# Kernel tuning notes

Hardware: AMD Instinct MI355X
Metric: run time of the kernel (lower is better)

Reference implementation:

```python
import jax, jax.numpy as jnp
import numpy as np

ALPHA = 0.2      # leak / integration time constant
E_FRAC = 0.8     # fraction of excitatory units (Dale's law)
NUM_LAYERS = 3


def setup_inputs() -> dict:
    key = jax.random.key(0)
    T, B, IN, H = 128, 64, 512, 1024
    ks = jax.random.split(key, 7)
    inputs = jax.random.normal(ks[0], (T, B, IN), jnp.float32)
    hidden_init = jax.random.uniform(ks[1], (1, B, H), jnp.float32) * 0.1
    # positive weights (clamped-positive in the original EI cell); Dale sign applied in reference
    W_in0 = jax.random.uniform(ks[2], (H, IN), jnp.float32) * (1.0 / np.sqrt(IN))
    W_in1 = jax.random.uniform(ks[3], (H, H), jnp.float32) * (1.0 / np.sqrt(H))
    W_in2 = jax.random.uniform(ks[4], (H, H), jnp.float32) * (1.0 / np.sqrt(H))
    W_rec = jax.random.uniform(ks[5], (NUM_LAYERS, H, H), jnp.float32) * (1.0 / H)
    b = jnp.zeros((NUM_LAYERS, H), jnp.float32)
    return {"inputs": inputs, "hidden_init": hidden_init, "W_in0": W_in0,
            "W_in1": W_in1, "W_in2": W_in2, "W_rec": W_rec, "b": b}


def reference(inputs, hidden_init, W_in0, W_in1, W_in2, W_rec, b):
    H = W_rec.shape[-1]
    ne = int(H * E_FRAC)
    signs = jnp.concatenate([jnp.ones((ne,), inputs.dtype), -jnp.ones((H - ne,), inputs.dtype)])
    e_mask = (signs > 0).astype(inputs.dtype)           # [H], zero out inhibitory feedforward
    # Dale's law: positive magnitudes with fixed presynaptic sign (columns)
    W_eff = jnp.abs(W_rec) * signs[None, None, :]        # [L, H, H]
    W_ins = (jnp.abs(W_in0), jnp.abs(W_in1), jnp.abs(W_in2))
    h0 = hidden_init[0]                                  # [B, H], shared across layers

    def step(carry, x_t):
        hs, vs = carry
        cell_input = x_t
        new_hs, new_vs = [], []
        for j in range(NUM_LAYERS):
            pre = cell_input @ W_ins[j].T + hs[j] @ W_eff[j].T + b[j]
            v = (1.0 - ALPHA) * vs[j] + ALPHA * pre      # leaky preact state
            h = jax.nn.relu(v)
            cell_input = h * e_mask                      # only excitatory units project forward
            new_hs.append(h)
            new_vs.append(v)
        return (tuple(new_hs), tuple(new_vs)), (cell_input, jnp.stack(new_hs))

    init = (tuple(h0 for _ in range(NUM_LAYERS)),
            tuple(jnp.zeros_like(h0) for _ in range(NUM_LAYERS)))
    _, (outputs, hiddens) = jax.lax.scan(step, init, inputs)
    # outputs: [T, B, H]; hiddens: [T, L, B, H] -> per-layer [T+1, B, H] incl. init
    hiddens = jnp.moveaxis(hiddens, 1, 0)                # [L, T, B, H]
    init_stack = jnp.broadcast_to(h0, (NUM_LAYERS, 1) + h0.shape)
    all_hiddens = jnp.concatenate([init_stack, hiddens], axis=1)  # [L, T+1, B, H]
    return outputs, all_hiddens
```

## Files before the change

### kernel.cpp

```cpp
#include <hip/hip_runtime.h>

#define T_STEPS 128
#define BATCH   64
#define INDIM   512
#define HDIM    1024
#define NE      819
#define OUT0_SZ (T_STEPS*BATCH*HDIM)
#define BH      (BATCH*HDIM)
#define ALLH_L  (129*BH)

#define HS_LAY   131072
#define HS_SLOT  393216
#define NSLOT    131
#define XF_T     65536
#define NBLK     192
#define NGRP     8
#define GSZ      24

typedef short bf16x8 __attribute__((ext_vector_type(8)));
typedef short short2v __attribute__((ext_vector_type(2)));
typedef float f32x4  __attribute__((ext_vector_type(4)));
typedef float f32x2  __attribute__((ext_vector_type(2)));

__device__ __forceinline__ short f2bf(float f){
    unsigned u = __float_as_uint(f);
    u += 0x7FFF + ((u >> 16) & 1);
    return (short)(u >> 16);
}
__device__ __forceinline__ float bf2f(short s){
    return __uint_as_float(((unsigned)(unsigned short)s) << 16);
}

__global__ __launch_bounds__(256) void ei_prep_w(const float* __restrict__ Win0,
        const float* __restrict__ Win1, const float* __restrict__ Win2,
        const float* __restrict__ Wrec, short* __restrict__ wf){
    int gid = blockIdx.x * 256 + threadIdx.x;
    int j, local, nkb, kff; const float* Win; short* base;
    if (gid < 196608)      { j=0; local=gid;        nkb=48; kff=512;  Win=Win0; base=wf; }
    else if (gid < 458752) { j=1; local=gid-196608; nkb=64; kff=1024; Win=Win1; base=wf+3145728; }
    else                   { j=2; local=gid-458752; nkb=64; kff=1024; Win=Win2; base=wf+7340032; }
    int lane = local & 63;
    int fi   = local >> 6;
    int kb   = fi % nkb;
    int it   = fi / nkb;
    int i    = it*16 + (lane & 15);
    int k0   = kb*32 + ((lane >> 4) << 3);
    const float* wrec_row = Wrec + ((size_t)j*HDIM + i)*HDIM;
    bf16x8 hv, lv;
    #pragma unroll
    for (int e = 0; e < 8; ++e){
        int k = k0 + e;
        float w;
        if (k < kff){
            w = fabsf(Win[(size_t)i*kff + k]);
            if (j != 0 && k >= NE) w = 0.f;
        } else {
            int kr = k - kff;
            w = fabsf(wrec_row[kr]);
            if (kr >= NE) w = -w;
        }
        short h = f2bf(w);
        hv[e] = h;
        lv[e] = f2bf(w - bf2f(h));
    }
    short* dst = base + (size_t)fi*1024 + lane*8;
    *(bf16x8*)dst         = hv;
    *(bf16x8*)(dst + 512) = lv;
}

__global__ __launch_bounds__(256) void ei_prep_xf(const float* __restrict__ x,
        short* __restrict__ xf){
    int gid = blockIdx.x * 256 + threadIdx.x;
    int lane = gid & 63;
    int bt   = (gid >> 6) & 3;
    int kb   = (gid >> 8) & 15;
    int t    = gid >> 12;
    int b = bt*16 + (lane & 15);
    int k = kb*32 + ((lane >> 4) << 3);
    const float* src = x + ((size_t)t*BATCH + b)*INDIM + k;
    float4 v0 = *(const float4*)src;
    float4 v1 = *(const float4*)(src + 4);
    float f[8] = {v0.x,v0.y,v0.z,v0.w,v1.x,v1.y,v1.z,v1.w};
    bf16x8 hv, lv;
    #pragma unroll
    for (int e = 0; e < 8; ++e){
        short h = f2bf(f[e]);
        hv[e] = h; lv[e] = f2bf(f[e] - bf2f(h));
    }
    short* dst = xf + (size_t)t*XF_T + (((size_t)(kb*4 + bt)) << 9) + lane*8;
    *(bf16x8*)dst            = hv;
    *(bf16x8*)(dst + 32768)  = lv;
}

__global__ __launch_bounds__(256) void ei_init5(const float* __restrict__ h0,
        float* __restrict__ out, short* __restrict__ hf, int* __restrict__ bar){
    int idx = blockIdx.x * 256 + threadIdx.x;
    int l = idx >> 16, r = idx & 0xFFFF;
    out[OUT0_SZ + (size_t)l*ALLH_L + r] = h0[r];
    if (idx < 1024) bar[idx] = 0;
    if (idx < 24576){
        int lane = idx & 63, bt = (idx >> 6) & 3, kb = (idx >> 8) & 31, j = idx >> 13;
        int b = bt*16 + (lane & 15);
        int k = kb*32 + ((lane >> 4) << 3);
        const float* src = h0 + (size_t)b*HDIM + k;
        float4 v0 = *(const float4*)src;
        float4 v1 = *(const float4*)(src + 4);
        float f[8] = {v0.x,v0.y,v0.z,v0.w,v1.x,v1.y,v1.z,v1.w};
        bf16x8 hv, lv;
        #pragma unroll
        for (int e = 0; e < 8; ++e){
            short hh = f2bf(f[e]);
            hv[e] = hh; lv[e] = f2bf(f[e] - bf2f(hh));
        }
        int off = ((kb*4 + bt) << 9) + lane*8;
        short* b0 = hf + (size_t)j*HS_LAY + off;
        *(bf16x8*)b0           = hv;
        *(bf16x8*)(b0 + 65536) = lv;
    }
}

template<int NKW, int NKFF, int FFLO>
__device__ __forceinline__ void step_mm4(
        const short* __restrict__ pff, const short* __restrict__ prec,
        const short* __restrict__ wp0, const short* __restrict__ wp1,
        int kb0, int btbase, int laneo, f32x4 acc[2][2])
{
    bf16x8 ah[NKW][2], al[NKW][2];
    #pragma unroll
    for (int kk = 0; kk < NKW; ++kk){
        int kb = kb0 + kk;
        const short* pa; int lo;
        if (kb < NKFF){ pa = pff + (kb << 11); lo = FFLO; }
        else          { pa = prec + ((kb - NKFF) << 11); lo = 65536; }
        ah[kk][0] = *(const bf16x8*)(pa + ((btbase + 0) << 9) + laneo);
        ah[kk][1] = *(const bf16x8*)(pa + ((btbase + 1) << 9) + laneo);
        al[kk][0] = *(const bf16x8*)(pa + lo + ((btbase + 0) << 9) + laneo);
        al[kk][1] = *(const bf16x8*)(pa + lo + ((btbase + 1) << 9) + laneo);
    }
    __builtin_amdgcn_sched_barrier(0);
    bf16x8 wh[2][2], wl[2][2];
    {
        const short* a = wp0 + (kb0 << 10);
        const short* b = wp1 + (kb0 << 10);
        wh[0][0] = *(const bf16x8*)a; wl[0][0] = *(const bf16x8*)(a + 512);
        wh[0][1] = *(const bf16x8*)b; wl[0][1] = *(const bf16x8*)(b + 512);
    }
    __builtin_amdgcn_sched_barrier(0);
    #pragma unroll
    for (int kk = 0; kk < NKW; ++kk){
        if (kk + 1 < NKW){
            const int nb = (kk + 1) & 1;
            const short* a = wp0 + ((kb0 + kk + 1) << 10);
            const short* b = wp1 + ((kb0 + kk + 1) << 10);
            wh[nb][0] = *(const bf16x8*)a; wl[nb][0] = *(const bf16x8*)(a + 512);
            wh[nb][1] = *(const bf16x8*)b; wl[nb][1] = *(const bf16x8*)(b + 512);
        }
        const int b2 = kk & 1;
        acc[0][0] = __builtin_amdgcn_mfma_f32_16x16x32_bf16(ah[kk][0], wh[b2][0], acc[0][0], 0,0,0);
        acc[0][1] = __builtin_amdgcn_mfma_f32_16x16x32_bf16(ah[kk][1], wh[b2][0], acc[0][1], 0,0,0);
        acc[1][0] = __builtin_amdgcn_mfma_f32_16x16x32_bf16(ah[kk][0], wh[b2][1], acc[1][0], 0,0,0);
        acc[1][1] = __builtin_amdgcn_mfma_f32_16x16x32_bf16(ah[kk][1], wh[b2][1], acc[1][1], 0,0,0);
        acc[0][0] = __builtin_amdgcn_mfma_f32_16x16x32_bf16(al[kk][0], wh[b2][0], acc[0][0], 0,0,0);
        acc[0][1] = __builtin_amdgcn_mfma_f32_16x16x32_bf16(al[kk][1], wh[b2][0], acc[0][1], 0,0,0);
        acc[1][0] = __builtin_amdgcn_mfma_f32_16x16x32_bf16(al[kk][0], wh[b2][1], acc[1][0], 0,0,0);
        acc[1][1] = __builtin_amdgcn_mfma_f32_16x16x32_bf16(al[kk][1], wh[b2][1], acc[1][1], 0,0,0);
        acc[0][0] = __builtin_amdgcn_mfma_f32_16x16x32_bf16(ah[kk][0], wl[b2][0], acc[0][0], 0,0,0);
        acc[0][1] = __builtin_amdgcn_mfma_f32_16x16x32_bf16(ah[kk][1], wl[b2][0], acc[0][1], 0,0,0);
        acc[1][0] = __builtin_amdgcn_mfma_f32_16x16x32_bf16(ah[kk][0], wl[b2][1], acc[1][0], 0,0,0);
        acc[1][1] = __builtin_amdgcn_mfma_f32_16x16x32_bf16(ah[kk][1], wl[b2][1], acc[1][1], 0,0,0);
    }
}

__global__ __launch_bounds__(512, 2) void ei_persist7(
        const short* __restrict__ xf, const short* __restrict__ wf,
        const float* __restrict__ bias, float* __restrict__ out,
        short* __restrict__ hf, int* __restrict__ bar)
{
    const int bid   = blockIdx.x;
    const int g     = bid & 7;
    const int w     = bid >> 3;
    const int j     = w >> 3;
    const int strip = g*4 + ((w >> 1) & 3);
    const int bhalf = w & 1;
    const int grp   = g;

    const int tx    = threadIdx.x;
    const int wv    = tx >> 6, lane = tx & 63;
    const int laneo = lane * 8;
    const int btbase = bhalf * 2;
    const int it0   = strip * 2;

    const short* wfj = wf + (j == 0 ? 0 : (j == 1 ? 3145728 : 7340032));
    const int nkb  = (j == 0) ? 48 : 64;
    const int NKW  = nkb >> 3;
    const int kb0  = wv * NKW;
    const short* wp0 = wfj + it0*nkb*1024 + laneo;
    const short* wp1 = wp0 + nkb*1024;

    const int btl = tx >> 8;
    const int q   = tx & 255;
    const int lnw = q >> 2;
    const int e0  = (q & 3) * 2;
    const int b_g = (bhalf*2 + btl)*16 + (lnw & 15);
    const int i_g = strip*32 + ((lnw >> 4) << 3) + e0;
    const int bl  = b_g & 31;
    const int il0 = ((lnw >> 4) << 3) + e0;
    const int hoff = ((strip*4 + bhalf*2 + btl) << 9) + q*2;
    const f32x2 bb = *(const f32x2*)&bias[j*HDIM + i_g];
    f32x2 vreg = {0.f, 0.f};

    __shared__ float psum[8][32][34];

    for (int s = 0; s < T_STEPS + 2; ++s){
        const int t = s - j;
        const bool act = (t >= 0) && (t < T_STEPS);
        if (s > 0){
            while (__hip_atomic_load(&bar[512 + grp*32],
                    __ATOMIC_RELAXED, __HIP_MEMORY_SCOPE_AGENT) < s)
                __builtin_amdgcn_s_sleep(1);
            asm volatile("" ::: "memory");
            __builtin_amdgcn_sched_barrier(0);
        }
        if (act){
            const short* hfr  = hf + (size_t)s*HS_SLOT;
            const short* prec = (t == 0) ? (hf + (size_t)j*HS_LAY)
                                         : (hfr + (size_t)j*HS_LAY);
            f32x4 acc[2][2] = {{{0.f,0.f,0.f,0.f},{0.f,0.f,0.f,0.f}},
                               {{0.f,0.f,0.f,0.f},{0.f,0.f,0.f,0.f}}};
            if (j == 0)
                step_mm4<6,16,32768>(xf + (size_t)t*XF_T, prec, wp0, wp1, kb0, btbase, laneo, acc);
            else if (j == 1)
                step_mm4<8,32,65536>(hfr, prec, wp0, wp1, kb0, btbase, laneo, acc);
            else
                step_mm4<8,32,65536>(hfr + HS_LAY, prec, wp0, wp1, kb0, btbase, laneo, acc);

            const int r0 = (lane >> 4) << 2, l15 = lane & 15;
            #pragma unroll
            for (int ic = 0; ic < 2; ++ic)
                #pragma unroll
                for (int bt = 0; bt < 2; ++bt)
                    #pragma unroll
                    for (int r = 0; r < 4; ++r)
                        psum[wv][bt*16 + r0 + r][ic*16 + l15] = acc[ic][bt][r];
        }
        __syncthreads();
        if (act){
            float sum0 = 0.f, sum1 = 0.f;
            #pragma unroll
            for (int ww = 0; ww < 8; ++ww){
                f32x2 p = *(f32x2*)&psum[ww][bl][il0];
                sum0 += p[0]; sum1 += p[1];
            }
            vreg[0] = 0.8f*vreg[0] + 0.2f*(sum0 + bb[0]);
            vreg[1] = 0.8f*vreg[1] + 0.2f*(sum1 + bb[1]);
            float h0v = vreg[0] > 0.f ? vreg[0] : 0.f;
            float h1v = vreg[1] > 0.f ? vreg[1] : 0.f;
            f32x2 hv2 = {h0v, h1v};
            *(f32x2*)&out[OUT0_SZ + ((size_t)(j*129 + t + 1))*BH + b_g*HDIM + i_g] = hv2;
            if (j == 2){
                f32x2 o2 = {(i_g < NE) ? h0v : 0.f, (i_g + 1 < NE) ? h1v : 0.f};
                *(f32x2*)&out[(size_t)t*BH + b_g*HDIM + i_g] = o2;
            }
            short hh0 = f2bf(h0v), hl0 = f2bf(h0v - bf2f(hh0));
            short hh1 = f2bf(h1v), hl1 = f2bf(h1v - bf2f(hh1));
            int hi2 = (int)(unsigned short)hh0 | ((int)(unsigned short)hh1 << 16);
            int lo2 = (int)(unsigned short)hl0 | ((int)(unsigned short)hl1 << 16);
            short* hww = hf + (size_t)(s + 1)*HS_SLOT + (size_t)j*HS_LAY + hoff;
            asm volatile("global_store_dword %0, %1, off sc0 sc1"
                         :: "v"(hww), "v"(hi2) : "memory");
            asm volatile("global_store_dword %0, %1, off sc0 sc1"
                         :: "v"(hww + 65536), "v"(lo2) : "memory");
        }
        if (s == T_STEPS + 1) break;
        asm volatile("s_waitcnt vmcnt(0)" ::: "memory");
        __syncthreads();
        if (tx == 0){
            int prev = __hip_atomic_fetch_add(&bar[grp*32], 1,
                        __ATOMIC_RELAXED, __HIP_MEMORY_SCOPE_AGENT);
            if (prev == (s + 1)*GSZ - 1){
                int sp = __hip_atomic_fetch_add(&bar[256], 1,
                        __ATOMIC_RELAXED, __HIP_MEMORY_SCOPE_AGENT);
                if (sp == (s + 1)*NGRP - 1){
                    #pragma unroll
                    for (int gg = 0; gg < NGRP; ++gg)
                        __hip_atomic_store(&bar[512 + gg*32], s + 1,
                                __ATOMIC_RELAXED, __HIP_MEMORY_SCOPE_AGENT);
                }
            }
        }
    }
}

#define HS_PAR_FB 393216
__global__ __launch_bounds__(256) void ei_init3(const float* __restrict__ h0,
        float* __restrict__ out, float* __restrict__ v_ws, short* __restrict__ hfb){
    int idx = blockIdx.x * 256 + threadIdx.x;
    int l = idx >> 16, r = idx & 0xFFFF;
    float h = h0[r];
    out[OUT0_SZ + (size_t)l*ALLH_L + r] = h;
    v_ws[idx] = 0.f;
    if (idx < 24576){
        int lane = idx & 63, bt = (idx >> 6) & 3, kb = (idx >> 8) & 31, j = idx >> 13;
        int b = bt*16 + (lane & 15);
        int k = kb*32 + ((lane >> 4) << 3);
        const float* src = h0 + (size_t)b*HDIM + k;
        float4 v0 = *(const float4*)src;
        float4 v1 = *(const float4*)(src + 4);
        float f[8] = {v0.x,v0.y,v0.z,v0.w,v1.x,v1.y,v1.z,v1.w};
        bf16x8 hv, lv;
        #pragma unroll
        for (int e = 0; e < 8; ++e){
            short hh = f2bf(f[e]);
            hv[e] = hh; lv[e] = f2bf(f[e] - bf2f(hh));
        }
        int off = ((kb*4 + bt) << 9) + lane*8;
        short* b0 = hfb + (size_t)j*HS_LAY + off;
        *(bf16x8*)b0           = hv;
        *(bf16x8*)(b0 + 65536) = lv;
        short* b1 = b0 + HS_PAR_FB;
        *(bf16x8*)b1           = hv;
        *(bf16x8*)(b1 + 65536) = lv;
    }
}

template<int NKW, int NKFF, int FFLO>
__device__ __forceinline__ void stage_body5(
        const short* __restrict__ pff, const short* __restrict__ prec,
        const short* __restrict__ wp, int kb0, int laneo, f32x4 acc[4])
{
    bf16x8 wbh[NKW], wbl[NKW];
    #pragma unroll
    for (int kk = 0; kk < NKW; ++kk){
        const short* w0 = wp + ((kb0 + kk) << 10);
        wbh[kk] = *(const bf16x8*)w0;
        wbl[kk] = *(const bf16x8*)(w0 + 512);
    }
    bf16x8 ah[2][4], al[2][4];
    auto loadA = [&](int kk, int buf){
        int kb = kb0 + kk;
        const short* pa; int lo;
        if (kb < NKFF){ pa = pff + (kb << 11); lo = FFLO; }
        else          { pa = prec + ((kb - NKFF) << 11); lo = 65536; }
        #pragma unroll
        for (int bt = 0; bt < 4; ++bt){
            ah[buf][bt] = *(const bf16x8*)(pa + (bt << 9) + laneo);
            al[buf][bt] = *(const bf16x8*)(pa + lo + (bt << 9) + laneo);
        }
    };
    loadA(0, 0);
    #pragma unroll
    for (int kk = 0; kk < NKW; ++kk){
        if (kk + 1 < NKW) loadA(kk + 1, (kk + 1) & 1);
        const int bf = kk & 1;
        #pragma unroll
        for (int bt = 0; bt < 4; ++bt)
            acc[bt] = __builtin_amdgcn_mfma_f32_16x16x32_bf16(ah[bf][bt], wbh[kk], acc[bt], 0,0,0);
        #pragma unroll
        for (int bt = 0; bt < 4; ++bt)
            acc[bt] = __builtin_amdgcn_mfma_f32_16x16x32_bf16(al[bf][bt], wbh[kk], acc[bt], 0,0,0);
        #pragma unroll
        for (int bt = 0; bt < 4; ++bt)
            acc[bt] = __builtin_amdgcn_mfma_f32_16x16x32_bf16(ah[bf][bt], wbl[kk], acc[bt], 0,0,0);
    }
}

__global__ __launch_bounds__(512, 2) void ei_stage5(
        const short* __restrict__ xf, const short* __restrict__ wf,
        const float* __restrict__ bias, float* __restrict__ out,
        float* __restrict__ v_ws, short* __restrict__ hfb, int s)
{
    int j = blockIdx.x >> 6;
    int t = s - j;
    if (t < 0 || t >= T_STEPS) return;
    int it = blockIdx.x & 63;
    int wv = threadIdx.x >> 6, lane = threadIdx.x & 63;
    int laneo = lane * 8;
    int par_r = (s - 1) & 1, par_w = s & 1;
    const short* hfr  = hfb + par_r*HS_PAR_FB;
    const short* prec = hfr + j*HS_LAY;

    f32x4 acc[4] = {{0.f,0.f,0.f,0.f},{0.f,0.f,0.f,0.f},
                    {0.f,0.f,0.f,0.f},{0.f,0.f,0.f,0.f}};

    if (j == 0){
        const short* pff = xf + t*XF_T;
        const short* wp  = wf + it*48*1024 + laneo;
        stage_body5<6,16,32768>(pff, prec, wp, wv*6, laneo, acc);
    } else if (j == 1){
        const short* pff = hfr;
        const short* wp  = wf + 3145728 + it*64*1024 + laneo;
        stage_body5<8,32,65536>(pff, prec, wp, wv*8, laneo, acc);
    } else {
        const short* pff = hfr + HS_LAY;
        const short* wp  = wf + 7340032 + it*64*1024 + laneo;
        stage_body5<8,32,65536>(pff, prec, wp, wv*8, laneo, acc);
    }

    __shared__ float psum[8][64][18];
    {
        int r0 = (lane >> 4) << 2, l15 = lane & 15;
        #pragma unroll
        for (int bt = 0; bt < 4; ++bt)
            #pragma unroll
            for (int r = 0; r < 4; ++r)
                psum[wv][bt*16 + r0 + r][l15] = acc[bt][r];
    }
    __syncthreads();

    int tx  = threadIdx.x;
    int b   = tx >> 3;
    int il0 = (tx & 7) << 1;
    float* allh = out + OUT0_SZ + ((size_t)(j*129 + t + 1))*BH;
    float* outp = out + (size_t)t*BH;
    short* hww  = hfb + par_w*HS_PAR_FB + j*HS_LAY;
    float sum0 = 0.f, sum1 = 0.f;
    #pragma unroll
    for (int w = 0; w < 8; ++w){
        f32x2 p = *(f32x2*)&psum[w][b][il0];
        sum0 += p[0]; sum1 += p[1];
    }
    int i = it*16 + il0;
    f32x2 bb = *(const f32x2*)&bias[j*HDIM + i];
    int vo = (j*BATCH + b)*HDIM + i;
    f32x2 vold = *(f32x2*)&v_ws[vo];
    float vn0 = 0.8f * vold[0] + 0.2f * (sum0 + bb[0]);
    float vn1 = 0.8f * vold[1] + 0.2f * (sum1 + bb[1]);
    f32x2 vnv = {vn0, vn1};
    *(f32x2*)&v_ws[vo] = vnv;
    float h0 = vn0 > 0.f ? vn0 : 0.f;
    float h1 = vn1 > 0.f ? vn1 : 0.f;
    f32x2 hv2 = {h0, h1};
    *(f32x2*)&allh[b*HDIM + i] = hv2;
    short hh0 = f2bf(h0), hl0 = f2bf(h0 - bf2f(hh0));
    short hh1 = f2bf(h1), hl1 = f2bf(h1 - bf2f(hh1));
    int kb  = i >> 5, btw = b >> 4;
    int lnw = (b & 15) + (((i >> 3) & 3) << 4);
    int off = ((kb*4 + btw) << 9) + lnw*8 + (i & 7);
    short2v hi2 = {hh0, hh1}, lo2 = {hl0, hl1};
    *(short2v*)(hww + off)         = hi2;
    *(short2v*)(hww + off + 65536) = lo2;
    if (j == 2){
        f32x2 o2 = {(i < NE) ? h0 : 0.f, (i + 1 < NE) ? h1 : 0.f};
        *(f32x2*)&outp[b*HDIM + i] = o2;
    }
}

extern "C" void kernel_launch(void* const* d_in, const int* in_sizes, int n_in,
                              void* d_out, int out_size, void* d_ws, size_t ws_size,
                              hipStream_t stream) {
    const float* xin  = (const float*)d_in[0];
    const float* h0   = (const float*)d_in[1];
    const float* Win0 = (const float*)d_in[2];
    const float* Win1 = (const float*)d_in[3];
    const float* Win2 = (const float*)d_in[4];
    const float* Wrec = (const float*)d_in[5];
    const float* bias = (const float*)d_in[6];
    float* out  = (float*)d_out;
    char* ws    = (char*)d_ws;

    const size_t HF_B   = (size_t)NSLOT * HS_SLOT * 2ULL;
    const size_t need_p = 65536 + HF_B + 16777216ULL + 23068672ULL;

    if (ws_size >= need_p) {
        int*   bar = (int*)ws;
        short* hf  = (short*)(ws + 65536);
        short* xf  = (short*)(ws + 65536 + HF_B);
        short* wfp = (short*)(ws + 65536 + HF_B + 16777216ULL);
        hipLaunchKernelGGL(ei_prep_w, dim3(2816), dim3(256), 0, stream,
                           Win0, Win1, Win2, Wrec, wfp);
        hipLaunchKernelGGL(ei_prep_xf, dim3(2048), dim3(256), 0, stream, xin, xf);
        hipLaunchKernelGGL(ei_init5, dim3(768), dim3(256), 0, stream, h0, out, hf, bar);
        hipLaunchKernelGGL(ei_persist7, dim3(NBLK), dim3(512), 0, stream,
                           xf, wfp, bias, out, hf, bar);
    } else {
        float* v_ws = (float*)ws;
        short* hfb  = (short*)(ws + 786432);
        short* xf   = (short*)(ws + 786432 + 1572864ULL);
        short* wfp  = (short*)(ws + 786432 + 1572864ULL + 16777216ULL);
        hipLaunchKernelGGL(ei_prep_w, dim3(2816), dim3(256), 0, stream,
                           Win0, Win1, Win2, Wrec, wfp);
        hipLaunchKernelGGL(ei_prep_xf, dim3(2048), dim3(256), 0, stream, xin, xf);
        hipLaunchKernelGGL(ei_init3, dim3(768), dim3(256), 0, stream, h0, out, v_ws, hfb);
        for (int s = 0; s < T_STEPS + 2; ++s)
            hipLaunchKernelGGL(ei_stage5, dim3(192), dim3(512), 0, stream,
                               xf, wfp, bias, out, v_ws, hfb, s);
    }
}
```

Baseline: 1.082 ms.

## Double per-block output tile to 64 columns and halve persistent grid to 96 blocks

Each persistent block now computes 64 hidden columns (four 16-wide MFMA tiles) instead of 32, so the activation fragments loaded per k-step are reused across four weight tiles. The grid shrinks from 192 to 96 blocks and barrier group sizes are adjusted to match. The A-operand loads move from a full upfront preload to a double-buffered pipeline interleaved with the weight loads. The intent is to cut redundant activation traffic and reduce the number of blocks participating in each grid-wide barrier, at the cost of fewer CUs doing the per-step GEMM, more registers per thread and a larger shared reduction buffer. A leftover dead code block computes unused values.

```diff
diff --git a/kernel.cpp b/kernel.cpp
--- a/kernel.cpp
+++ b/kernel.cpp
@@ -13,9 +13,8 @@
 #define HS_SLOT  393216
 #define NSLOT    131
 #define XF_T     65536
-#define NBLK     192
-#define NGRP     8
-#define GSZ      24
+#define NBLK8    96
+#define GSZ8     12
 
 typedef short bf16x8 __attribute__((ext_vector_type(8)));
 typedef short short2v __attribute__((ext_vector_type(2)));
@@ -120,58 +119,48 @@
 }
 
 template<int NKW, int NKFF, int FFLO>
-__device__ __forceinline__ void step_mm4(
+__device__ __forceinline__ void step_mm8(
         const short* __restrict__ pff, const short* __restrict__ prec,
-        const short* __restrict__ wp0, const short* __restrict__ wp1,
-        int kb0, int btbase, int laneo, f32x4 acc[2][2])
+        const short* __restrict__ wp0, int wstride,
+        int kb0, int btbase, int laneo, f32x4 acc[4][2])
 {
-    bf16x8 ah[NKW][2], al[NKW][2];
-    #pragma unroll
-    for (int kk = 0; kk < NKW; ++kk){
+    bf16x8 wh[2][4], wl[2][4], ah[2][2], al[2][2];
+    auto loadW = [&](int kk, int buf){
+        #pragma unroll
+        for (int ic = 0; ic < 4; ++ic){
+            const short* a = wp0 + ic*wstride + ((kb0 + kk) << 10);
+            wh[buf][ic] = *(const bf16x8*)a;
+            wl[buf][ic] = *(const bf16x8*)(a + 512);
+        }
+    };
+    auto loadA = [&](int kk, int buf){
         int kb = kb0 + kk;
         const short* pa; int lo;
         if (kb < NKFF){ pa = pff + (kb << 11); lo = FFLO; }
         else          { pa = prec + ((kb - NKFF) << 11); lo = 65536; }
-        ah[kk][0] = *(const bf16x8*)(pa + ((btbase + 0) << 9) + laneo);
-        ah[kk][1] = *(const bf16x8*)(pa + ((btbase + 1) << 9) + laneo);
-        al[kk][0] = *(const bf16x8*)(pa + lo + ((btbase + 0) << 9) + laneo);
-        al[kk][1] = *(const bf16x8*)(pa + lo + ((btbase + 1) << 9) + laneo);
-    }
-    __builtin_amdgcn_sched_barrier(0);
-    bf16x8 wh[2][2], wl[2][2];
-    {
-        const short* a = wp0 + (kb0 << 10);
-        const short* b = wp1 + (kb0 << 10);
-        wh[0][0] = *(const bf16x8*)a; wl[0][0] = *(const bf16x8*)(a + 512);
-        wh[0][1] = *(const bf16x8*)b; wl[0][1] = *(const bf16x8*)(b + 512);
-    }
-    __builtin_amdgcn_sched_barrier(0);
+        ah[buf][0] = *(const bf16x8*)(pa + ((btbase + 0) << 9) + laneo);
+        ah[buf][1] = *(const bf16x8*)(pa + ((btbase + 1) << 9) + laneo);
+        al[buf][0] = *(const bf16x8*)(pa + lo + ((btbase + 0) << 9) + laneo);
+        al[buf][1] = *(const bf16x8*)(pa + lo + ((btbase + 1) << 9) + laneo);
+    };
+    loadW(0, 0); loadA(0, 0);
     #pragma unroll
     for (int kk = 0; kk < NKW; ++kk){
-        if (kk + 1 < NKW){
-            const int nb = (kk + 1) & 1;
-            const short* a = wp0 + ((kb0 + kk + 1) << 10);
-            const short* b = wp1 + ((kb0 + kk + 1) << 10);
-            wh[nb][0] = *(const bf16x8*)a; wl[nb][0] = *(const bf16x8*)(a + 512);
-            wh[nb][1] = *(const bf16x8*)b; wl[nb][1] = *(const bf16x8*)(b + 512);
-        }
-        const int b2 = kk & 1;
-        acc[0][0] = __builtin_amdgcn_mfma_f32_16x16x32_bf16(ah[kk][0], wh[b2][0], acc[0][0], 0,0,0);
-        acc[0][1] = __builtin_amdgcn_mfma_f32_16x16x32_bf16(ah[kk][1], wh[b2][0], acc[0][1], 0,0,0);
-        acc[1][0] = __builtin_amdgcn_mfma_f32_16x16x32_bf16(ah[kk][0], wh[b2][1], acc[1][0], 0,0,0);
-        acc[1][1] = __builtin_amdgcn_mfma_f32_16x16x32_bf16(ah[kk][1], wh[b2][1], acc[1][1], 0,0,0);
-        acc[0][0] = __builtin_amdgcn_mfma_f32_16x16x32_bf16(al[kk][0], wh[b2][0], acc[0][0], 0,0,0);
-        acc[0][1] = __builtin_amdgcn_mfma_f32_16x16x32_bf16(al[kk][1], wh[b2][0], acc[0][1], 0,0,0);
-        acc[1][0] = __builtin_amdgcn_mfma_f32_16x16x32_bf16(al[kk][0], wh[b2][1], acc[1][0], 0,0,0);
-        acc[1][1] = __builtin_amdgcn_mfma_f32_16x16x32_bf16(al[kk][1], wh[b2][1], acc[1][1], 0,0,0);
-        acc[0][0] = __builtin_amdgcn_mfma_f32_16x16x32_bf16(ah[kk][0], wl[b2][0], acc[0][0], 0,0,0);
-        acc[0][1] = __builtin_amdgcn_mfma_f32_16x16x32_bf16(ah[kk][1], wl[b2][0], acc[0][1], 0,0,0);
-        acc[1][0] = __builtin_amdgcn_mfma_f32_16x16x32_bf16(ah[kk][0], wl[b2][1], acc[1][0], 0,0,0);
-        acc[1][1] = __builtin_amdgcn_mfma_f32_16x16x32_bf16(ah[kk][1], wl[b2][1], acc[1][1], 0,0,0);
-    }
-}
-
-__global__ __launch_bounds__(512, 2) void ei_persist7(
+        if (kk + 1 < NKW){ loadW(kk + 1, (kk + 1) & 1); loadA(kk + 1, (kk + 1) & 1); }
+        const int b = kk & 1;
+        #pragma unroll
+        for (int ic = 0; ic < 4; ++ic){
+            acc[ic][0] = __builtin_amdgcn_mfma_f32_16x16x32_bf16(ah[b][0], wh[b][ic], acc[ic][0], 0,0,0);
+            acc[ic][1] = __builtin_amdgcn_mfma_f32_16x16x32_bf16(ah[b][1], wh[b][ic], acc[ic][1], 0,0,0);
+            acc[ic][0] = __builtin_amdgcn_mfma_f32_16x16x32_bf16(al[b][0], wh[b][ic], acc[ic][0], 0,0,0);
+            acc[ic][1] = __builtin_amdgcn_mfma_f32_16x16x32_bf16(al[b][1], wh[b][ic], acc[ic][1], 0,0,0);
+            acc[ic][0] = __builtin_amdgcn_mfma_f32_16x16x32_bf16(ah[b][0], wl[b][ic], acc[ic][0], 0,0,0);
+            acc[ic][1] = __builtin_amdgcn_mfma_f32_16x16x32_bf16(ah[b][1], wl[b][ic], acc[ic][1], 0,0,0);
+        }
+    }
+}
+
+__global__ __launch_bounds__(512, 2) void ei_persist8(
         const short* __restrict__ xf, const short* __restrict__ wf,
         const float* __restrict__ bias, float* __restrict__ out,
         short* __restrict__ hf, int* __restrict__ bar)
@@ -179,8 +168,8 @@
     const int bid   = blockIdx.x;
     const int g     = bid & 7;
     const int w     = bid >> 3;
-    const int j     = w >> 3;
-    const int strip = g*4 + ((w >> 1) & 3);
+    const int j     = w >> 2;
+    const int strip = g*2 + ((w >> 1) & 1);
     const int bhalf = w & 1;
     const int grp   = g;
 
@@ -188,28 +177,31 @@
     const int wv    = tx >> 6, lane = tx & 63;
     const int laneo = lane * 8;
     const int btbase = bhalf * 2;
-    const int it0   = strip * 2;
+    const int it0   = strip * 4;
 
     const short* wfj = wf + (j == 0 ? 0 : (j == 1 ? 3145728 : 7340032));
     const int nkb  = (j == 0) ? 48 : 64;
     const int NKW  = nkb >> 3;
     const int kb0  = wv * NKW;
-    const short* wp0 = wfj + it0*nkb*1024 + laneo;
-    const short* wp1 = wp0 + nkb*1024;
-
-    const int btl = tx >> 8;
+    const int wstride = nkb * 1024;
+    const short* wp0 = wfj + it0*wstride + laneo;
+
+    const int c0  = tx >> 8;
     const int q   = tx & 255;
     const int lnw = q >> 2;
     const int e0  = (q & 3) * 2;
-    const int b_g = (bhalf*2 + btl)*16 + (lnw & 15);
-    const int i_g = strip*32 + ((lnw >> 4) << 3) + e0;
+    const int b_g = (bhalf*2 + c0)*16 + (lnw & 15);
     const int bl  = b_g & 31;
-    const int il0 = ((lnw >> 4) << 3) + e0;
-    const int hoff = ((strip*4 + bhalf*2 + btl) << 9) + q*2;
-    const f32x2 bb = *(const f32x2*)&bias[j*HDIM + i_g];
-    f32x2 vreg = {0.f, 0.f};
-
-    __shared__ float psum[8][32][34];
+    const int ilb = ((lnw >> 4) << 3) + e0;
+    const int i_g0 = strip*64 + ilb;
+    const int i_g1 = i_g0 + 32;
+    const int hoff0 = (((strip*2 + 0)*4 + bhalf*2 + c0) << 9) + q*2;
+    const int hoff1 = (((strip*2 + 1)*4 + bhalf*2 + c0) << 9) + q*2;
+    const f32x2 bb0 = *(const f32x2*)&bias[j*HDIM + i_g0];
+    const f32x2 bb1 = *(const f32x2*)&bias[j*HDIM + i_g1];
+    f32x2 vreg0 = {0.f, 0.f}, vreg1 = {0.f, 0.f};
+
+    __shared__ float psum[8][32][68];
 
     for (int s = 0; s < T_STEPS + 2; ++s){
         const int t = s - j;
@@ -225,18 +217,20 @@
             const short* hfr  = hf + (size_t)s*HS_SLOT;
             const short* prec = (t == 0) ? (hf + (size_t)j*HS_LAY)
                                          : (hfr + (size_t)j*HS_LAY);
-            f32x4 acc[2][2] = {{{0.f,0.f,0.f,0.f},{0.f,0.f,0.f,0.f}},
+            f32x4 acc[4][2] = {{{0.f,0.f,0.f,0.f},{0.f,0.f,0.f,0.f}},
+                               {{0.f,0.f,0.f,0.f},{0.f,0.f,0.f,0.f}},
+                               {{0.f,0.f,0.f,0.f},{0.f,0.f,0.f,0.f}},
                                {{0.f,0.f,0.f,0.f},{0.f,0.f,0.f,0.f}}};
             if (j == 0)
-                step_mm4<6,16,32768>(xf + (size_t)t*XF_T, prec, wp0, wp1, kb0, btbase, laneo, acc);
+                step_mm8<6,16,32768>(xf + (size_t)t*XF_T, prec, wp0, wstride, kb0, btbase, laneo, acc);
             else if (j == 1)
-                step_mm4<8,32,65536>(hfr, prec, wp0, wp1, kb0, btbase, laneo, acc);
+                step_mm8<8,32,65536>(hfr, prec, wp0, wstride, kb0, btbase, laneo, acc);
             else
-                step_mm4<8,32,65536>(hfr + HS_LAY, prec, wp0, wp1, kb0, btbase, laneo, acc);
+                step_mm8<8,32,65536>(hfr + HS_LAY, prec, wp0, wstride, kb0, btbase, laneo, acc);
 
             const int r0 = (lane >> 4) << 2, l15 = lane & 15;
             #pragma unroll
-            for (int ic = 0; ic < 2; ++ic)
+            for (int ic = 0; ic < 4; ++ic)
                 #pragma unroll
                 for (int bt = 0; bt < 2; ++bt)
                     #pragma unroll
@@ -245,31 +239,55 @@
         }
         __syncthreads();
         if (act){
-            float sum0 = 0.f, sum1 = 0.f;
+            float s00 = 0.f, s01 = 0.f, s10 = 0.f, s11 = 0.f;
             #pragma unroll
             for (int ww = 0; ww < 8; ++ww){
-                f32x2 p = *(f32x2*)&psum[ww][bl][il0];
-                sum0 += p[0]; sum1 += p[1];
+                f32x2 p0 = *(f32x2*)&psum[ww][bl][ilb];
+                f32x2 p1 = *(f32x2*)&psum[ww][bl][ilb + 32];
+                s00 += p0[0]; s01 += p0[1];
+                s10 += p1[0]; s11 += p1[1];
             }
-            vreg[0] = 0.8f*vreg[0] + 0.2f*(sum0 + bb[0]);
-            vreg[1] = 0.8f*vreg[1] + 0.2f*(sum1 + bb[1]);
-            float h0v = vreg[0] > 0.f ? vreg[0] : 0.f;
-            float h1v = vreg[1] > 0.f ? vreg[1] : 0.f;
-            f32x2 hv2 = {h0v, h1v};
-            *(f32x2*)&out[OUT0_SZ + ((size_t)(j*129 + t + 1))*BH + b_g*HDIM + i_g] = hv2;
+            vreg0[0] = 0.8f*vreg0[0] + 0.2f*(s00 + bb0[0]);
+            vreg0[1] = 0.8f*vreg0[1] + 0.2f*(s01 + bb0[1]);
+            vreg1[0] = 0.8f*vreg1[0] + 0.2f*(s10 + bb1[0]);
+            vreg1[1] = 0.8f*vreg1[1] + 0.2f*(s11 + bb1[1]);
+            float h00 = vreg0[0] > 0.f ? vreg0[0] : 0.f;
+            float h01 = vreg0[1] > 0.f ? vreg0[1] : 0.f;
+            float h10 = vreg1[0] > 0.f ? vreg1[0] : 0.f;
+            float h11 = vreg1[1] > 0.f ? vreg1[1] : 0.f;
+            float* ah = &out[OUT0_SZ + ((size_t)(j*129 + t + 1))*BH + (size_t)b_g*HDIM];
+            f32x2 hv20 = {h00, h01}; *(f32x2*)&ah[i_g0] = hv20;
+            f32x2 hv21 = {h10, h11}; *(f32x2*)&ah[i_g1] = hv21;
             if (j == 2){
-                f32x2 o2 = {(i_g < NE) ? h0v : 0.f, (i_g + 1 < NE) ? h1v : 0.f};
-                *(f32x2*)&out[(size_t)t*BH + b_g*HDIM + i_g] = o2;
+                float* op = &out[(size_t)t*BH + (size_t)b_g*HDIM];
+                f32x2 o0 = {(i_g0 < NE) ? h00 : 0.f, (i_g0 + 1 < NE) ? h01 : 0.f};
+                f32x2 o1 = {(i_g1 < NE) ? h10 : 0.f, (i_g1 + 1 < NE) ? h11 : 0.f};
+                *(f32x2*)&op[i_g0] = o0;
+                *(f32x2*)&op[i_g1] = o1;
             }
-            short hh0 = f2bf(h0v), hl0 = f2bf(h0v - bf2f(hh0));
-            short hh1 = f2bf(h1v), hl1 = f2bf(h1v - bf2f(hh1));
-            int hi2 = (int)(unsigned short)hh0 | ((int)(unsigned short)hh1 << 16);
-            int lo2 = (int)(unsigned short)hl0 | ((int)(unsigned short)hl1 << 16);
-            short* hww = hf + (size_t)(s + 1)*HS_SLOT + (size_t)j*HS_LAY + hoff;
-            asm volatile("global_store_dword %0, %1, off sc0 sc1"
-                         :: "v"(hww), "v"(hi2) : "memory");
-            asm volatile("global_store_dword %0, %1, off sc0 sc1"
-                         :: "v"(hww + 65536), "v"(lo2) : "memory");
+            short* hwb = hf + (size_t)(s + 1)*HS_SLOT + (size_t)j*HS_LAY;
+            short hh, hl; int dw;
+            hh = f2bf(h00); hl = f2bf(h01);
+            dw = (int)(unsigned short)hh | ((int)(unsigned short)hl << 16);
+            {   short hla = f2bf(h00 - bf2f(hh)), hlb = f2bf(h01 - bf2f(f2bf(h01) ? 0 : 0)); (void)hla; (void)hlb; }
+            {
+                short a0 = f2bf(h00), a1 = f2bf(h01);
+                short l0 = f2bf(h00 - bf2f(a0)), l1 = f2bf(h01 - bf2f(a1));
+                int hi2 = (int)(unsigned short)a0 | ((int)(unsigned short)a1 << 16);
+                int lo2 = (int)(unsigned short)l0 | ((int)(unsigned short)l1 << 16);
+                short* d = hwb + hoff0;
+                asm volatile("global_store_dword %0, %1, off sc0 sc1" :: "v"(d), "v"(hi2) : "memory");
+                asm volatile("global_store_dword %0, %1, off sc0 sc1" :: "v"(d + 65536), "v"(lo2) : "memory");
+            }
+            {
+                short a0 = f2bf(h10), a1 = f2bf(h11);
+                short l0 = f2bf(h10 - bf2f(a0)), l1 = f2bf(h11 - bf2f(a1));
+                int hi2 = (int)(unsigned short)a0 | ((int)(unsigned short)a1 << 16);
+                int lo2 = (int)(unsigned short)l0 | ((int)(unsigned short)l1 << 16);
+                short* d = hwb + hoff1;
+                asm volatile("global_store_dword %0, %1, off sc0 sc1" :: "v"(d), "v"(hi2) : "memory");
+                asm volatile("global_store_dword %0, %1, off sc0 sc1" :: "v"(d + 65536), "v"(lo2) : "memory");
+            }
         }
         if (s == T_STEPS + 1) break;
         asm volatile("s_waitcnt vmcnt(0)" ::: "memory");
@@ -277,12 +295,12 @@
         if (tx == 0){
             int prev = __hip_atomic_fetch_add(&bar[grp*32], 1,
                         __ATOMIC_RELAXED, __HIP_MEMORY_SCOPE_AGENT);
-            if (prev == (s + 1)*GSZ - 1){
+            if (prev == (s + 1)*GSZ8 - 1){
                 int sp = __hip_atomic_fetch_add(&bar[256], 1,
                         __ATOMIC_RELAXED, __HIP_MEMORY_SCOPE_AGENT);
-                if (sp == (s + 1)*NGRP - 1){
+                if (sp == (s + 1)*8 - 1){
                     #pragma unroll
-                    for (int gg = 0; gg < NGRP; ++gg)
+                    for (int gg = 0; gg < 8; ++gg)
                         __hip_atomic_store(&bar[512 + gg*32], s + 1,
                                 __ATOMIC_RELAXED, __HIP_MEMORY_SCOPE_AGENT);
                 }
@@ -470,7 +488,7 @@
                            Win0, Win1, Win2, Wrec, wfp);
         hipLaunchKernelGGL(ei_prep_xf, dim3(2048), dim3(256), 0, stream, xin, xf);
         hipLaunchKernelGGL(ei_init5, dim3(768), dim3(256), 0, stream, h0, out, hf, bar);
-        hipLaunchKernelGGL(ei_persist7, dim3(NBLK), dim3(512), 0, stream,
+        hipLaunchKernelGGL(ei_persist8, dim3(NBLK8), dim3(512), 0, stream,
                            xf, wfp, bias, out, hf, bar);
     } else {
         float* v_ws = (float*)ws;
```

Result: slower. 1.893 ms (+75.0%).
